# Optimization experiments

Measured on AMD Instinct MI355X. Metric: run time of the kernel, lower is better.

Reference implementation:

```python
import jax, jax.numpy as jnp
import numpy as np

NEG_SLOPE = 0.01  # torch F.leaky_relu default

def leaky_relu(x):
    return jnp.where(x >= 0, x, NEG_SLOPE * x)

def setup_inputs() -> dict:
    key = jax.random.key(0)
    ks = jax.random.split(key, 16)
    N, D, H, L = 2048, 512, 256, 16
    # normalized-adjacency-like matrix: row sums ~0.5 to keep activations sane
    A_hat = jax.random.uniform(ks[0], (N, N), dtype=jnp.float32) / N
    X = jax.random.normal(ks[1], (N, D), dtype=jnp.float32)
    eps = jax.random.normal(ks[2], (N, L), dtype=jnp.float32)
    def lin(k, fan_out, fan_in):
        s = 1.0 / np.sqrt(fan_in)
        kw, kb = jax.random.split(k)
        W = jax.random.uniform(kw, (fan_out, fan_in), minval=-s, maxval=s, dtype=jnp.float32)
        b = jax.random.uniform(kb, (fan_out,), minval=-s, maxval=s, dtype=jnp.float32)
        return W, b
    W1, b1 = lin(ks[3], H, D)          # gcn1
    Wmu, bmu = lin(ks[4], L, H)        # gcn2_mu
    Wlv, blv = lin(ks[5], L, H)        # gcn2_logvar
    Wd1, bd1 = lin(ks[6], 2 * L, 2 * L)  # decoder_fc1
    Wd2, bd2 = lin(ks[7], 1, 2 * L)      # decoder_fc2
    return {"A_hat": A_hat, "X": X, "eps": eps,
            "W1": W1, "b1": b1, "Wmu": Wmu, "bmu": bmu,
            "Wlv": Wlv, "blv": blv, "Wd1": Wd1, "bd1": bd1,
            "Wd2": Wd2, "bd2": bd2}

def reference(A_hat, X, eps, W1, b1, Wmu, bmu, Wlv, blv, Wd1, bd1, Wd2, bd2):
    L = Wmu.shape[0]
    # --- encode: two GCN layers (A_hat @ X) @ W.T + b ---
    Hh = leaky_relu((A_hat @ X) @ W1.T + b1)           # [N, H]
    AH = A_hat @ Hh                                    # [N, H]
    mu = AH @ Wmu.T + bmu                              # [N, L]
    logvar = AH @ Wlv.T + blv                          # [N, L]
    # --- reparameterize ---
    Z = mu + eps * jnp.exp(0.5 * logvar)               # [N, L]
    # --- decode: pairwise MLP on concat(Z_i, Z_j), vectorized ---
    # fc1(concat(Zi,Zj)) = Zi @ Wd1[:, :L].T + Zj @ Wd1[:, L:].T + bd1
    P = Z @ Wd1[:, :L].T                               # [N, 2L]
    Q = Z @ Wd1[:, L:].T                               # [N, 2L]
    h = leaky_relu(P[:, None, :] + Q[None, :, :] + bd1)  # [N, N, 2L]
    A_pred = jax.nn.sigmoid(jnp.einsum('nmh,h->nm', h, Wd2[0]) + bd2[0])  # [N, N]
    return (A_pred, mu, logvar)
```

## Files before the change

kernel.cpp:

```cpp
#include <hip/hip_runtime.h>

#define NNODE 2048
#define DD    512
#define HHID  256
#define LLAT  16
#define H2    32

typedef __attribute__((ext_vector_type(8))) short  short8;
typedef __attribute__((ext_vector_type(4))) float  f32x4;

__device__ __forceinline__ unsigned short f2bf(float x) {
    unsigned int u = __float_as_uint(x);
    unsigned int r = (u + 0x7fffu + ((u >> 16) & 1u)) >> 16;
    return (unsigned short)r;
}
__device__ __forceinline__ float bf2f(unsigned short u) {
    return __uint_as_float(((unsigned int)u) << 16);
}

__global__ __launch_bounds__(256) void t0_cvt(const float* __restrict__ A,
                                              const float* __restrict__ X,
                                              const float* __restrict__ W1,
                                              unsigned short* __restrict__ Abf,
                                              unsigned short* __restrict__ Xbf,
                                              unsigned short* __restrict__ W1bf) {
    const int NT = 1343488;
    for (int v = blockIdx.x * 256 + threadIdx.x; v < NT; v += gridDim.x * 256) {
        const float* src; unsigned short* dst; int off;
        if (v < 1048576)      { src = A;  dst = Abf;  off = v; }
        else if (v < 1310720) { src = X;  dst = Xbf;  off = v - 1048576; }
        else                  { src = W1; dst = W1bf; off = v - 1310720; }
        float4 f = ((const float4*)src)[off];
        short4 h;
        h.x = (short)f2bf(f.x); h.y = (short)f2bf(f.y);
        h.z = (short)f2bf(f.z); h.w = (short)f2bf(f.w);
        ((short4*)dst)[off] = h;
    }
}

__global__ __launch_bounds__(256) void t1_mfma(const unsigned short* __restrict__ W1bf,
                                               const unsigned short* __restrict__ Xbf,
                                               float* __restrict__ XWp) {
    __shared__ __align__(16) unsigned short Ab[64][40];
    __shared__ __align__(16) unsigned short Bb[64][40];
    const int tid = threadIdx.x;
    const int n0 = blockIdx.x * 64;
    const int h0 = blockIdx.y * 64;
    const int ks = blockIdx.z;
    const int lane = tid & 63, wave = tid >> 6;
    const int wm = wave >> 1, wn = wave & 1;
    const int lm = lane & 15, lk = (lane >> 4) * 8;
    const int sr = tid >> 2, sc = (tid & 3) * 8;
    f32x4 acc[2][2] = {};
    for (int it = 0; it < 4; ++it) {
        int kk = ks * 128 + it * 32;
        *(uint4*)&Ab[sr][sc] = *(const uint4*)(W1bf + (size_t)(h0 + sr) * DD + kk + sc);
        *(uint4*)&Bb[sr][sc] = *(const uint4*)(Xbf  + (size_t)(n0 + sr) * DD + kk + sc);
        __syncthreads();
        short8 a0 = *(const short8*)&Ab[wm * 32 + lm][lk];
        short8 a1 = *(const short8*)&Ab[wm * 32 + 16 + lm][lk];
        short8 b0 = *(const short8*)&Bb[wn * 32 + lm][lk];
        short8 b1 = *(const short8*)&Bb[wn * 32 + 16 + lm][lk];
        acc[0][0] = __builtin_amdgcn_mfma_f32_16x16x32_bf16(a0, b0, acc[0][0], 0, 0, 0);
        acc[0][1] = __builtin_amdgcn_mfma_f32_16x16x32_bf16(a0, b1, acc[0][1], 0, 0, 0);
        acc[1][0] = __builtin_amdgcn_mfma_f32_16x16x32_bf16(a1, b0, acc[1][0], 0, 0, 0);
        acc[1][1] = __builtin_amdgcn_mfma_f32_16x16x32_bf16(a1, b1, acc[1][1], 0, 0, 0);
        __syncthreads();
    }
    float* outp = XWp + (size_t)ks * 524288;
    #pragma unroll
    for (int mi = 0; mi < 2; ++mi)
        #pragma unroll
        for (int ni = 0; ni < 2; ++ni)
            #pragma unroll
            for (int r = 0; r < 4; ++r) {
                int row = h0 + wm * 32 + mi * 16 + (lane >> 4) * 4 + r;
                int col = n0 + wn * 32 + ni * 16 + lm;
                outp[(size_t)row * NNODE + col] = acc[mi][ni][r];
            }
}

__global__ __launch_bounds__(256) void t1r(const float* __restrict__ XWp,
                                           unsigned short* __restrict__ XWt) {
    int v = blockIdx.x * 256 + threadIdx.x;
    const float4* p = (const float4*)XWp;
    float4 a = p[v];
    float4 b = p[v + 131072];
    float4 c = p[v + 262144];
    float4 d = p[v + 393216];
    float4 s;
    s.x = (a.x + b.x) + (c.x + d.x);
    s.y = (a.y + b.y) + (c.y + d.y);
    s.z = (a.z + b.z) + (c.z + d.z);
    s.w = (a.w + b.w) + (c.w + d.w);
    short4 h;
    h.x = (short)f2bf(s.x); h.y = (short)f2bf(s.y);
    h.z = (short)f2bf(s.z); h.w = (short)f2bf(s.w);
    ((short4*)XWt)[v] = h;
}

__global__ __launch_bounds__(256) void t2_mfma(const unsigned short* __restrict__ Abf,
                                               const unsigned short* __restrict__ XWt,
                                               float* __restrict__ Hp) {
    __shared__ __align__(16) unsigned short Ab[64][40];
    __shared__ __align__(16) unsigned short Bb[64][40];
    const int tid = threadIdx.x;
    const int m0 = blockIdx.x * 64;
    const int n0 = blockIdx.y * 64;
    const int ks = blockIdx.z;
    const int lane = tid & 63, wave = tid >> 6;
    const int wm = wave >> 1, wn = wave & 1;
    const int lm = lane & 15, lk = (lane >> 4) * 8;
    const int sr = tid >> 2, sc = (tid & 3) * 8;
    f32x4 acc[2][2] = {};
    for (int it = 0; it < 16; ++it) {
        int kk = ks * 512 + it * 32;
        *(uint4*)&Ab[sr][sc] = *(const uint4*)(Abf + (size_t)(m0 + sr) * NNODE + kk + sc);
        *(uint4*)&Bb[sr][sc] = *(const uint4*)(XWt + (size_t)(n0 + sr) * NNODE + kk + sc);
        __syncthreads();
        short8 a0 = *(const short8*)&Ab[wm * 32 + lm][lk];
        short8 a1 = *(const short8*)&Ab[wm * 32 + 16 + lm][lk];
        short8 b0 = *(const short8*)&Bb[wn * 32 + lm][lk];
        short8 b1 = *(const short8*)&Bb[wn * 32 + 16 + lm][lk];
        acc[0][0] = __builtin_amdgcn_mfma_f32_16x16x32_bf16(a0, b0, acc[0][0], 0, 0, 0);
        acc[0][1] = __builtin_amdgcn_mfma_f32_16x16x32_bf16(a0, b1, acc[0][1], 0, 0, 0);
        acc[1][0] = __builtin_amdgcn_mfma_f32_16x16x32_bf16(a1, b0, acc[1][0], 0, 0, 0);
        acc[1][1] = __builtin_amdgcn_mfma_f32_16x16x32_bf16(a1, b1, acc[1][1], 0, 0, 0);
        __syncthreads();
    }
    float* outp = Hp + (size_t)ks * 524288;
    #pragma unroll
    for (int mi = 0; mi < 2; ++mi)
        #pragma unroll
        for (int ni = 0; ni < 2; ++ni)
            #pragma unroll
            for (int r = 0; r < 4; ++r) {
                int row = m0 + wm * 32 + mi * 16 + (lane >> 4) * 4 + r;
                int col = n0 + wn * 32 + ni * 16 + lm;
                outp[(size_t)row * HHID + col] = acc[mi][ni][r];
            }
}

__global__ __launch_bounds__(256) void t2r(const float* __restrict__ Hp,
                                           const float* __restrict__ b1,
                                           unsigned short* __restrict__ Hbf) {
    int v = blockIdx.x * 256 + threadIdx.x;
    const float4* p = (const float4*)Hp;
    float4 a = p[v];
    float4 b = p[v + 131072];
    float4 c = p[v + 262144];
    float4 d = p[v + 393216];
    int dcol = (v & 63) * 4;
    float4 bb = *(const float4*)(b1 + dcol);
    float4 s;
    s.x = (a.x + b.x) + (c.x + d.x) + bb.x;
    s.y = (a.y + b.y) + (c.y + d.y) + bb.y;
    s.z = (a.z + b.z) + (c.z + d.z) + bb.z;
    s.w = (a.w + b.w) + (c.w + d.w) + bb.w;
    s.x = fmaxf(s.x, 0.01f * s.x);
    s.y = fmaxf(s.y, 0.01f * s.y);
    s.z = fmaxf(s.z, 0.01f * s.z);
    s.w = fmaxf(s.w, 0.01f * s.w);
    short4 h;
    h.x = (short)f2bf(s.x); h.y = (short)f2bf(s.y);
    h.z = (short)f2bf(s.z); h.w = (short)f2bf(s.w);
    ((short4*)Hbf)[v] = h;
}

__global__ __launch_bounds__(256) void t3_g(const unsigned short* __restrict__ Hbf,
                                            const float* __restrict__ Wmu,
                                            const float* __restrict__ Wlv,
                                            unsigned short* __restrict__ Gt) {
    __shared__ float Hs[8][260];
    __shared__ float Ws[32][260];
    const int tid = threadIdx.x;
    const int n0 = blockIdx.x * 8;
    #pragma unroll
    for (int s = 0; s < 8; ++s) {
        int idx = tid + s * 256;
        int row = idx >> 6, c = (idx & 63) * 4;
        const float* src = (row < 16) ? (Wmu + (size_t)row * HHID)
                                      : (Wlv + (size_t)(row - 16) * HHID);
        *(float4*)&Ws[row][c] = *(const float4*)(src + c);
    }
    {
        int r = tid >> 5, seg = tid & 31;
        int d = seg * 8;
        ushort4 u0 = *(const ushort4*)(Hbf + (size_t)(n0 + r) * HHID + d);
        ushort4 u1 = *(const ushort4*)(Hbf + (size_t)(n0 + r) * HHID + d + 4);
        Hs[r][d + 0] = bf2f(u0.x); Hs[r][d + 1] = bf2f(u0.y);
        Hs[r][d + 2] = bf2f(u0.z); Hs[r][d + 3] = bf2f(u0.w);
        Hs[r][d + 4] = bf2f(u1.x); Hs[r][d + 5] = bf2f(u1.y);
        Hs[r][d + 6] = bf2f(u1.z); Hs[r][d + 7] = bf2f(u1.w);
    }
    __syncthreads();
    const int r = tid >> 5, j = tid & 31;
    float acc = 0.f;
    #pragma unroll 8
    for (int d4 = 0; d4 < 64; ++d4) {
        float4 a = *(const float4*)&Hs[r][d4 * 4];
        float4 b = *(const float4*)&Ws[j][d4 * 4];
        acc += a.x * b.x + a.y * b.y + a.z * b.z + a.w * b.w;
    }
    Gt[(size_t)j * NNODE + n0 + r] = f2bf(acc);
}

__global__ __launch_bounds__(256) void t4_mfma(const unsigned short* __restrict__ Abf,
                                               const unsigned short* __restrict__ Gt,
                                               float* __restrict__ Mp) {
    __shared__ __align__(16) unsigned short Ab[64][40];
    __shared__ __align__(16) unsigned short Bb[32][40];
    const int tid = threadIdx.x;
    const int m0 = blockIdx.x * 64;
    const int ks = blockIdx.y;
    const int lane = tid & 63, wave = tid >> 6;
    const int lm = lane & 15, lk = (lane >> 4) * 8;
    const int sr = tid >> 2, sc = (tid & 3) * 8;
    f32x4 acc[2] = {};
    for (int it = 0; it < 8; ++it) {
        int kk = ks * 256 + it * 32;
        *(uint4*)&Ab[sr][sc] = *(const uint4*)(Abf + (size_t)(m0 + sr) * NNODE + kk + sc);
        if (tid < 128) {
            int row = tid >> 2, c = (tid & 3) * 8;
            *(uint4*)&Bb[row][c] = *(const uint4*)(Gt + (size_t)row * NNODE + kk + c);
        }
        __syncthreads();
        short8 a  = *(const short8*)&Ab[wave * 16 + lm][lk];
        short8 b0 = *(const short8*)&Bb[lm][lk];
        short8 b1 = *(const short8*)&Bb[16 + lm][lk];
        acc[0] = __builtin_amdgcn_mfma_f32_16x16x32_bf16(a, b0, acc[0], 0, 0, 0);
        acc[1] = __builtin_amdgcn_mfma_f32_16x16x32_bf16(a, b1, acc[1], 0, 0, 0);
        __syncthreads();
    }
    float* outp = Mp + (size_t)ks * 65536;
    #pragma unroll
    for (int ni = 0; ni < 2; ++ni)
        #pragma unroll
        for (int r = 0; r < 4; ++r) {
            int row = m0 + wave * 16 + (lane >> 4) * 4 + r;
            int col = ni * 16 + lm;
            outp[(size_t)row * H2 + col] = acc[ni][r];
        }
}

__global__ __launch_bounds__(256) void t5_z(const float* __restrict__ Mp,
                                            const float* __restrict__ bmu,
                                            const float* __restrict__ blv,
                                            const float* __restrict__ eps,
                                            const float* __restrict__ Wd1,
                                            const float* __restrict__ bd1,
                                            const float* __restrict__ Wd2,
                                            float* __restrict__ out_mu,
                                            float* __restrict__ out_lv,
                                            float* __restrict__ Pp,
                                            float* __restrict__ Qq,
                                            float* __restrict__ WP,
                                            float* __restrict__ WQ) {
    __shared__ float Zs[16][16];
    __shared__ float Psh[16][32];
    __shared__ float Qsh[16][32];
    const int tid = threadIdx.x;
    const int n0 = blockIdx.x * 16;
    {
        int nl = tid >> 4, l = tid & 15;
        int n = n0 + nl;
        float m = bmu[l], lv = blv[l];
        #pragma unroll
        for (int s = 0; s < 8; ++s) {
            m  += Mp[(size_t)s * 65536 + (size_t)n * H2 + l];
            lv += Mp[(size_t)s * 65536 + (size_t)n * H2 + 16 + l];
        }
        out_mu[(size_t)n * LLAT + l] = m;
        out_lv[(size_t)n * LLAT + l] = lv;
        Zs[nl][l] = m + eps[(size_t)n * LLAT + l] * __expf(0.5f * lv);
    }
    __syncthreads();
    #pragma unroll
    for (int p = 0; p < 2; ++p) {
        int idx = tid + p * 256;
        int nl = idx >> 5, o = idx & 31;
        int n = n0 + nl;
        float ap = bd1[o], aq = 0.f;
        #pragma unroll
        for (int l = 0; l < 16; ++l) {
            float z = Zs[nl][l];
            ap = fmaf(z, Wd1[o * H2 + l],      ap);
            aq = fmaf(z, Wd1[o * H2 + 16 + l], aq);
        }
        Pp[(size_t)n * H2 + o] = ap;
        Qq[(size_t)n * H2 + o] = aq;
        Psh[nl][o] = ap;
        Qsh[nl][o] = aq;
    }
    __syncthreads();
    if (tid < 32) {
        int nl = tid & 15, sel = tid >> 4;
        float a = 0.f;
        if (sel == 0) {
            #pragma unroll
            for (int o = 0; o < 32; ++o) a = fmaf(Wd2[o], Psh[nl][o], a);
            WP[n0 + nl] = a;
        } else {
            #pragma unroll
            for (int o = 0; o < 32; ++o) a = fmaf(Wd2[o], Qsh[nl][o], a);
            WQ[n0 + nl] = a;
        }
    }
}

__global__ __launch_bounds__(256) void t6_dec(const float* __restrict__ Pp,
                                              const float* __restrict__ Qq,
                                              const float* __restrict__ WP,
                                              const float* __restrict__ WQ,
                                              const float* __restrict__ Wd2,
                                              const float* __restrict__ bd2,
                                              float* __restrict__ Apred) {
    __shared__ float Qt[32][68];
    __shared__ float Ws2[32];
    __shared__ float WQs[64];
    const int tid = threadIdx.x;
    const int j0 = blockIdx.x * 64, i0 = blockIdx.y * 16;
    #pragma unroll
    for (int s = 0; s < 8; ++s) {
        int idx = tid + s * 256;
        int j = idx >> 5, o = idx & 31;
        Qt[o][j] = Qq[(size_t)(j0 + j) * H2 + o];
    }
    if (tid < 32) Ws2[tid] = Wd2[tid];
    if (tid >= 64 && tid < 128) WQs[tid - 64] = WQ[j0 + tid - 64];
    const int i = i0 + (tid >> 4);
    const int jq = tid & 15;
    float p[32];
    const float4* P4 = (const float4*)(Pp + (size_t)i * H2);
    #pragma unroll
    for (int c = 0; c < 8; ++c) {
        float4 v = P4[c];
        p[c * 4] = v.x; p[c * 4 + 1] = v.y; p[c * 4 + 2] = v.z; p[c * 4 + 3] = v.w;
    }
    const float WPi = WP[i];
    __syncthreads();
    f32x4 acc = {0.f, 0.f, 0.f, 0.f};
    #pragma unroll
    for (int o = 0; o < 32; ++o) {
        float4 q = *(const float4*)&Qt[o][jq * 4];
        float w = Ws2[o], po = p[o];
        acc[0] = fmaf(w, fabsf(po + q.x), acc[0]);
        acc[1] = fmaf(w, fabsf(po + q.y), acc[1]);
        acc[2] = fmaf(w, fabsf(po + q.z), acc[2]);
        acc[3] = fmaf(w, fabsf(po + q.w), acc[3]);
    }
    float4 wq = *(const float4*)&WQs[jq * 4];
    const float base = fmaf(0.505f, WPi, bd2[0]);
    float4 r;
    float l0 = fmaf(0.505f, wq.x, fmaf(0.495f, acc[0], base));
    float l1 = fmaf(0.505f, wq.y, fmaf(0.495f, acc[1], base));
    float l2 = fmaf(0.505f, wq.z, fmaf(0.495f, acc[2], base));
    float l3 = fmaf(0.505f, wq.w, fmaf(0.495f, acc[3], base));
    r.x = 1.f / (1.f + __expf(-l0));
    r.y = 1.f / (1.f + __expf(-l1));
    r.z = 1.f / (1.f + __expf(-l2));
    r.w = 1.f / (1.f + __expf(-l3));
    *(float4*)(Apred + (size_t)i * NNODE + j0 + jq * 4) = r;
}

extern "C" void kernel_launch(void* const* d_in, const int* in_sizes, int n_in,
                              void* d_out, int out_size, void* d_ws, size_t ws_size,
                              hipStream_t stream) {
    const float* A   = (const float*)d_in[0];
    const float* X   = (const float*)d_in[1];
    const float* eps = (const float*)d_in[2];
    const float* W1  = (const float*)d_in[3];
    const float* b1  = (const float*)d_in[4];
    const float* Wmu = (const float*)d_in[5];
    const float* bmu = (const float*)d_in[6];
    const float* Wlv = (const float*)d_in[7];
    const float* blv = (const float*)d_in[8];
    const float* Wd1 = (const float*)d_in[9];
    const float* bd1 = (const float*)d_in[10];
    const float* Wd2 = (const float*)d_in[11];
    const float* bd2 = (const float*)d_in[12];
    float* out = (float*)d_out;
    char* ws = (char*)d_ws;

    unsigned short* Abf  = (unsigned short*)(ws);
    unsigned short* Xbf  = (unsigned short*)(ws + 8388608);
    unsigned short* W1bf = (unsigned short*)(ws + 10485760);
    float*          XWp  = (float*)(ws + 10747904);
    unsigned short* XWt  = (unsigned short*)(ws + 19136512);
    float*          Hp   = (float*)(ws + 20185088);
    unsigned short* Hbf  = (unsigned short*)(ws + 28573696);
    unsigned short* Gt   = (unsigned short*)(ws + 29622272);
    float*          Mp   = (float*)(ws + 29753344);
    float*          Pp   = (float*)(ws + 31850496);
    float*          Qq   = (float*)(ws + 32112640);
    float*          WP   = (float*)(ws + 32374784);
    float*          WQ   = (float*)(ws + 32382976);

    float* out_mu = out + (size_t)NNODE * NNODE;
    float* out_lv = out_mu + NNODE * LLAT;

    t0_cvt <<<2048,            256, 0, stream>>>(A, X, W1, Abf, Xbf, W1bf);
    t1_mfma<<<dim3(32, 4, 4),  256, 0, stream>>>(W1bf, Xbf, XWp);
    t1r    <<<512,             256, 0, stream>>>(XWp, XWt);
    t2_mfma<<<dim3(32, 4, 4),  256, 0, stream>>>(Abf, XWt, Hp);
    t2r    <<<512,             256, 0, stream>>>(Hp, b1, Hbf);
    t3_g   <<<256,             256, 0, stream>>>(Hbf, Wmu, Wlv, Gt);
    t4_mfma<<<dim3(32, 8),     256, 0, stream>>>(Abf, Gt, Mp);
    t5_z   <<<128,             256, 0, stream>>>(Mp, bmu, blv, eps, Wd1, bd1, Wd2,
                                                 out_mu, out_lv, Pp, Qq, WP, WQ);
    t6_dec <<<dim3(32, 128),   256, 0, stream>>>(Pp, Qq, WP, WQ, Wd2, bd2, out);
}
```

Baseline: 141.2 us.

## Fuse conversion into GEMMs, drop split-K reductions, add register prefetch

The X and W1 bf16 conversion is folded into the X·W1 GEMM, which now runs without split-K and writes bf16 XWt directly. The A conversion runs in extra blocks of the same launch. The second GEMM now covers the full K range with 64-wide k-steps and applies bias plus leaky-relu in its epilogue, so the partial-sum buffers and the t1r/t2r reduction kernels go away. Global loads in k2_h and k4_m are prefetched into registers one step ahead. This cuts three launches and several MB of fp32 partial traffic, at the cost of fewer blocks per GEMM and therefore lower parallelism.

```diff
diff --git a/kernel.cpp b/kernel.cpp
--- a/kernel.cpp
+++ b/kernel.cpp
@@ -18,44 +18,53 @@
     return __uint_as_float(((unsigned int)u) << 16);
 }
 
-__global__ __launch_bounds__(256) void t0_cvt(const float* __restrict__ A,
-                                              const float* __restrict__ X,
-                                              const float* __restrict__ W1,
-                                              unsigned short* __restrict__ Abf,
-                                              unsigned short* __restrict__ Xbf,
-                                              unsigned short* __restrict__ W1bf) {
-    const int NT = 1343488;
-    for (int v = blockIdx.x * 256 + threadIdx.x; v < NT; v += gridDim.x * 256) {
-        const float* src; unsigned short* dst; int off;
-        if (v < 1048576)      { src = A;  dst = Abf;  off = v; }
-        else if (v < 1310720) { src = X;  dst = Xbf;  off = v - 1048576; }
-        else                  { src = W1; dst = W1bf; off = v - 1310720; }
-        float4 f = ((const float4*)src)[off];
-        short4 h;
-        h.x = (short)f2bf(f.x); h.y = (short)f2bf(f.y);
-        h.z = (short)f2bf(f.z); h.w = (short)f2bf(f.w);
-        ((short4*)dst)[off] = h;
-    }
-}
-
-__global__ __launch_bounds__(256) void t1_mfma(const unsigned short* __restrict__ W1bf,
-                                               const unsigned short* __restrict__ Xbf,
-                                               float* __restrict__ XWp) {
+__global__ __launch_bounds__(256) void k1_cvt_xw(const float* __restrict__ A,
+                                                 const float* __restrict__ X,
+                                                 const float* __restrict__ W1,
+                                                 unsigned short* __restrict__ Abf,
+                                                 unsigned short* __restrict__ XWt) {
+    const int tid = threadIdx.x;
+    if (blockIdx.x >= 128) {
+        for (int v = (blockIdx.x - 128) * 256 + tid; v < 1048576; v += 32768) {
+            float4 f = ((const float4*)A)[v];
+            short4 h;
+            h.x = (short)f2bf(f.x); h.y = (short)f2bf(f.y);
+            h.z = (short)f2bf(f.z); h.w = (short)f2bf(f.w);
+            ((short4*)Abf)[v] = h;
+        }
+        return;
+    }
     __shared__ __align__(16) unsigned short Ab[64][40];
     __shared__ __align__(16) unsigned short Bb[64][40];
-    const int tid = threadIdx.x;
-    const int n0 = blockIdx.x * 64;
-    const int h0 = blockIdx.y * 64;
-    const int ks = blockIdx.z;
+    const int h0 = (blockIdx.x & 3) * 64;
+    const int n0 = (blockIdx.x >> 2) * 64;
     const int lane = tid & 63, wave = tid >> 6;
     const int wm = wave >> 1, wn = wave & 1;
     const int lm = lane & 15, lk = (lane >> 4) * 8;
     const int sr = tid >> 2, sc = (tid & 3) * 8;
     f32x4 acc[2][2] = {};
-    for (int it = 0; it < 4; ++it) {
-        int kk = ks * 128 + it * 32;
-        *(uint4*)&Ab[sr][sc] = *(const uint4*)(W1bf + (size_t)(h0 + sr) * DD + kk + sc);
-        *(uint4*)&Bb[sr][sc] = *(const uint4*)(Xbf  + (size_t)(n0 + sr) * DD + kk + sc);
+    for (int it = 0; it < 16; ++it) {
+        int kk = it * 32;
+        {
+            const float* ap = W1 + (size_t)(h0 + sr) * DD + kk + sc;
+            float4 f0 = *(const float4*)ap;
+            float4 f1 = *(const float4*)(ap + 4);
+            short8 h;
+            h[0] = (short)f2bf(f0.x); h[1] = (short)f2bf(f0.y);
+            h[2] = (short)f2bf(f0.z); h[3] = (short)f2bf(f0.w);
+            h[4] = (short)f2bf(f1.x); h[5] = (short)f2bf(f1.y);
+            h[6] = (short)f2bf(f1.z); h[7] = (short)f2bf(f1.w);
+            *(short8*)&Ab[sr][sc] = h;
+            const float* bp = X + (size_t)(n0 + sr) * DD + kk + sc;
+            float4 g0 = *(const float4*)bp;
+            float4 g1 = *(const float4*)(bp + 4);
+            short8 g;
+            g[0] = (short)f2bf(g0.x); g[1] = (short)f2bf(g0.y);
+            g[2] = (short)f2bf(g0.z); g[3] = (short)f2bf(g0.w);
+            g[4] = (short)f2bf(g1.x); g[5] = (short)f2bf(g1.y);
+            g[6] = (short)f2bf(g1.z); g[7] = (short)f2bf(g1.w);
+            *(short8*)&Bb[sr][sc] = g;
+        }
         __syncthreads();
         short8 a0 = *(const short8*)&Ab[wm * 32 + lm][lk];
         short8 a1 = *(const short8*)&Ab[wm * 32 + 16 + lm][lk];
@@ -67,7 +76,6 @@
         acc[1][1] = __builtin_amdgcn_mfma_f32_16x16x32_bf16(a1, b1, acc[1][1], 0, 0, 0);
         __syncthreads();
     }
-    float* outp = XWp + (size_t)ks * 524288;
     #pragma unroll
     for (int mi = 0; mi < 2; ++mi)
         #pragma unroll
@@ -76,95 +84,63 @@
             for (int r = 0; r < 4; ++r) {
                 int row = h0 + wm * 32 + mi * 16 + (lane >> 4) * 4 + r;
                 int col = n0 + wn * 32 + ni * 16 + lm;
-                outp[(size_t)row * NNODE + col] = acc[mi][ni][r];
+                XWt[(size_t)row * NNODE + col] = f2bf(acc[mi][ni][r]);
             }
 }
 
-__global__ __launch_bounds__(256) void t1r(const float* __restrict__ XWp,
-                                           unsigned short* __restrict__ XWt) {
-    int v = blockIdx.x * 256 + threadIdx.x;
-    const float4* p = (const float4*)XWp;
-    float4 a = p[v];
-    float4 b = p[v + 131072];
-    float4 c = p[v + 262144];
-    float4 d = p[v + 393216];
-    float4 s;
-    s.x = (a.x + b.x) + (c.x + d.x);
-    s.y = (a.y + b.y) + (c.y + d.y);
-    s.z = (a.z + b.z) + (c.z + d.z);
-    s.w = (a.w + b.w) + (c.w + d.w);
-    short4 h;
-    h.x = (short)f2bf(s.x); h.y = (short)f2bf(s.y);
-    h.z = (short)f2bf(s.z); h.w = (short)f2bf(s.w);
-    ((short4*)XWt)[v] = h;
-}
-
-__global__ __launch_bounds__(256) void t2_mfma(const unsigned short* __restrict__ Abf,
-                                               const unsigned short* __restrict__ XWt,
-                                               float* __restrict__ Hp) {
-    __shared__ __align__(16) unsigned short Ab[64][40];
-    __shared__ __align__(16) unsigned short Bb[64][40];
+__global__ __launch_bounds__(256) void k2_h(const unsigned short* __restrict__ Abf,
+                                            const unsigned short* __restrict__ XWt,
+                                            const float* __restrict__ bias1,
+                                            unsigned short* __restrict__ Hbf) {
+    __shared__ __align__(16) unsigned short Ab[64][72];
+    __shared__ __align__(16) unsigned short Bb[32][72];
     const int tid = threadIdx.x;
     const int m0 = blockIdx.x * 64;
-    const int n0 = blockIdx.y * 64;
-    const int ks = blockIdx.z;
+    const int h0 = blockIdx.y * 32;
     const int lane = tid & 63, wave = tid >> 6;
-    const int wm = wave >> 1, wn = wave & 1;
     const int lm = lane & 15, lk = (lane >> 4) * 8;
-    const int sr = tid >> 2, sc = (tid & 3) * 8;
-    f32x4 acc[2][2] = {};
-    for (int it = 0; it < 16; ++it) {
-        int kk = ks * 512 + it * 32;
-        *(uint4*)&Ab[sr][sc] = *(const uint4*)(Abf + (size_t)(m0 + sr) * NNODE + kk + sc);
-        *(uint4*)&Bb[sr][sc] = *(const uint4*)(XWt + (size_t)(n0 + sr) * NNODE + kk + sc);
-        __syncthreads();
-        short8 a0 = *(const short8*)&Ab[wm * 32 + lm][lk];
-        short8 a1 = *(const short8*)&Ab[wm * 32 + 16 + lm][lk];
-        short8 b0 = *(const short8*)&Bb[wn * 32 + lm][lk];
-        short8 b1 = *(const short8*)&Bb[wn * 32 + 16 + lm][lk];
-        acc[0][0] = __builtin_amdgcn_mfma_f32_16x16x32_bf16(a0, b0, acc[0][0], 0, 0, 0);
-        acc[0][1] = __builtin_amdgcn_mfma_f32_16x16x32_bf16(a0, b1, acc[0][1], 0, 0, 0);
-        acc[1][0] = __builtin_amdgcn_mfma_f32_16x16x32_bf16(a1, b0, acc[1][0], 0, 0, 0);
-        acc[1][1] = __builtin_amdgcn_mfma_f32_16x16x32_bf16(a1, b1, acc[1][1], 0, 0, 0);
-        __syncthreads();
-    }
-    float* outp = Hp + (size_t)ks * 524288;
-    #pragma unroll
-    for (int mi = 0; mi < 2; ++mi)
-        #pragma unroll
-        for (int ni = 0; ni < 2; ++ni)
-            #pragma unroll
-            for (int r = 0; r < 4; ++r) {
-                int row = m0 + wm * 32 + mi * 16 + (lane >> 4) * 4 + r;
-                int col = n0 + wn * 32 + ni * 16 + lm;
-                outp[(size_t)row * HHID + col] = acc[mi][ni][r];
-            }
-}
-
-__global__ __launch_bounds__(256) void t2r(const float* __restrict__ Hp,
-                                           const float* __restrict__ b1,
-                                           unsigned short* __restrict__ Hbf) {
-    int v = blockIdx.x * 256 + threadIdx.x;
-    const float4* p = (const float4*)Hp;
-    float4 a = p[v];
-    float4 b = p[v + 131072];
-    float4 c = p[v + 262144];
-    float4 d = p[v + 393216];
-    int dcol = (v & 63) * 4;
-    float4 bb = *(const float4*)(b1 + dcol);
-    float4 s;
-    s.x = (a.x + b.x) + (c.x + d.x) + bb.x;
-    s.y = (a.y + b.y) + (c.y + d.y) + bb.y;
-    s.z = (a.z + b.z) + (c.z + d.z) + bb.z;
-    s.w = (a.w + b.w) + (c.w + d.w) + bb.w;
-    s.x = fmaxf(s.x, 0.01f * s.x);
-    s.y = fmaxf(s.y, 0.01f * s.y);
-    s.z = fmaxf(s.z, 0.01f * s.z);
-    s.w = fmaxf(s.w, 0.01f * s.w);
-    short4 h;
-    h.x = (short)f2bf(s.x); h.y = (short)f2bf(s.y);
-    h.z = (short)f2bf(s.z); h.w = (short)f2bf(s.w);
-    ((short4*)Hbf)[v] = h;
+    const int sr = tid >> 2, sc = (tid & 3) * 16;
+    const int br = tid >> 3, bc = (tid & 7) * 8;
+    f32x4 acc[2] = {};
+    const unsigned short* aA = Abf + (size_t)(m0 + sr) * NNODE + sc;
+    const unsigned short* aB = XWt + (size_t)(h0 + br) * NNODE + bc;
+    uint4 ra0 = *(const uint4*)(aA);
+    uint4 ra1 = *(const uint4*)(aA + 8);
+    uint4 rb  = *(const uint4*)(aB);
+    for (int it = 0; it < 32; ++it) {
+        *(uint4*)&Ab[sr][sc]     = ra0;
+        *(uint4*)&Ab[sr][sc + 8] = ra1;
+        *(uint4*)&Bb[br][bc]     = rb;
+        __syncthreads();
+        if (it < 31) {
+            int kk = (it + 1) * 64;
+            ra0 = *(const uint4*)(aA + kk);
+            ra1 = *(const uint4*)(aA + kk + 8);
+            rb  = *(const uint4*)(aB + kk);
+        }
+        #pragma unroll
+        for (int ko = 0; ko < 2; ++ko) {
+            short8 a  = *(const short8*)&Ab[wave * 16 + lm][ko * 32 + lk];
+            short8 b0 = *(const short8*)&Bb[lm][ko * 32 + lk];
+            short8 b1 = *(const short8*)&Bb[16 + lm][ko * 32 + lk];
+            acc[0] = __builtin_amdgcn_mfma_f32_16x16x32_bf16(a, b0, acc[0], 0, 0, 0);
+            acc[1] = __builtin_amdgcn_mfma_f32_16x16x32_bf16(a, b1, acc[1], 0, 0, 0);
+        }
+        __syncthreads();
+    }
+    const int q = lane >> 4;
+    #pragma unroll
+    for (int ni = 0; ni < 2; ++ni) {
+        int col = h0 + ni * 16 + lm;
+        float bb = bias1[col];
+        #pragma unroll
+        for (int r = 0; r < 4; ++r) {
+            int row = m0 + wave * 16 + q * 4 + r;
+            float s = acc[ni][r] + bb;
+            s = fmaxf(s, 0.01f * s);
+            Hbf[(size_t)row * HHID + col] = f2bf(s);
+        }
+    }
 }
 
 __global__ __launch_bounds__(256) void t3_g(const unsigned short* __restrict__ Hbf,
@@ -205,9 +181,9 @@
     Gt[(size_t)j * NNODE + n0 + r] = f2bf(acc);
 }
 
-__global__ __launch_bounds__(256) void t4_mfma(const unsigned short* __restrict__ Abf,
-                                               const unsigned short* __restrict__ Gt,
-                                               float* __restrict__ Mp) {
+__global__ __launch_bounds__(256) void k4_m(const unsigned short* __restrict__ Abf,
+                                            const unsigned short* __restrict__ Gt,
+                                            float* __restrict__ Mp) {
     __shared__ __align__(16) unsigned short Ab[64][40];
     __shared__ __align__(16) unsigned short Bb[32][40];
     const int tid = threadIdx.x;
@@ -217,14 +193,23 @@
     const int lm = lane & 15, lk = (lane >> 4) * 8;
     const int sr = tid >> 2, sc = (tid & 3) * 8;
     f32x4 acc[2] = {};
+    const int kbase = ks * 256;
+    const unsigned short* aA = Abf + (size_t)(m0 + sr) * NNODE + kbase + sc;
+    const unsigned short* aB = Gt;
+    uint4 ra = *(const uint4*)aA;
+    uint4 rb = {};
+    if (tid < 128) {
+        aB = Gt + (size_t)(tid >> 2) * NNODE + kbase + (tid & 3) * 8;
+        rb = *(const uint4*)aB;
+    }
     for (int it = 0; it < 8; ++it) {
-        int kk = ks * 256 + it * 32;
-        *(uint4*)&Ab[sr][sc] = *(const uint4*)(Abf + (size_t)(m0 + sr) * NNODE + kk + sc);
-        if (tid < 128) {
-            int row = tid >> 2, c = (tid & 3) * 8;
-            *(uint4*)&Bb[row][c] = *(const uint4*)(Gt + (size_t)row * NNODE + kk + c);
-        }
-        __syncthreads();
+        *(uint4*)&Ab[sr][sc] = ra;
+        if (tid < 128) *(uint4*)&Bb[tid >> 2][(tid & 3) * 8] = rb;
+        __syncthreads();
+        if (it < 7) {
+            ra = *(const uint4*)(aA + (it + 1) * 32);
+            if (tid < 128) rb = *(const uint4*)(aB + (it + 1) * 32);
+        }
         short8 a  = *(const short8*)&Ab[wave * 16 + lm][lk];
         short8 b0 = *(const short8*)&Bb[lm][lk];
         short8 b1 = *(const short8*)&Bb[16 + lm][lk];
@@ -382,31 +367,24 @@
     float* out = (float*)d_out;
     char* ws = (char*)d_ws;
 
-    unsigned short* Abf  = (unsigned short*)(ws);
-    unsigned short* Xbf  = (unsigned short*)(ws + 8388608);
-    unsigned short* W1bf = (unsigned short*)(ws + 10485760);
-    float*          XWp  = (float*)(ws + 10747904);
-    unsigned short* XWt  = (unsigned short*)(ws + 19136512);
-    float*          Hp   = (float*)(ws + 20185088);
-    unsigned short* Hbf  = (unsigned short*)(ws + 28573696);
-    unsigned short* Gt   = (unsigned short*)(ws + 29622272);
-    float*          Mp   = (float*)(ws + 29753344);
-    float*          Pp   = (float*)(ws + 31850496);
-    float*          Qq   = (float*)(ws + 32112640);
-    float*          WP   = (float*)(ws + 32374784);
-    float*          WQ   = (float*)(ws + 32382976);
+    unsigned short* Abf = (unsigned short*)(ws);
+    unsigned short* XWt = (unsigned short*)(ws + 8388608);
+    unsigned short* Hbf = (unsigned short*)(ws + 9437184);
+    unsigned short* Gt  = (unsigned short*)(ws + 10485760);
+    float*          Mp  = (float*)(ws + 10616832);
+    float*          Pp  = (float*)(ws + 12713984);
+    float*          Qq  = (float*)(ws + 12976128);
+    float*          WP  = (float*)(ws + 13238272);
+    float*          WQ  = (float*)(ws + 13246464);
 
     float* out_mu = out + (size_t)NNODE * NNODE;
     float* out_lv = out_mu + NNODE * LLAT;
 
-    t0_cvt <<<2048,            256, 0, stream>>>(A, X, W1, Abf, Xbf, W1bf);
-    t1_mfma<<<dim3(32, 4, 4),  256, 0, stream>>>(W1bf, Xbf, XWp);
-    t1r    <<<512,             256, 0, stream>>>(XWp, XWt);
-    t2_mfma<<<dim3(32, 4, 4),  256, 0, stream>>>(Abf, XWt, Hp);
-    t2r    <<<512,             256, 0, stream>>>(Hp, b1, Hbf);
-    t3_g   <<<256,             256, 0, stream>>>(Hbf, Wmu, Wlv, Gt);
-    t4_mfma<<<dim3(32, 8),     256, 0, stream>>>(Abf, Gt, Mp);
-    t5_z   <<<128,             256, 0, stream>>>(Mp, bmu, blv, eps, Wd1, bd1, Wd2,
+    k1_cvt_xw<<<256,           256, 0, stream>>>(A, X, W1, Abf, XWt);
+    k2_h     <<<dim3(32, 8),   256, 0, stream>>>(Abf, XWt, b1, Hbf);
+    t3_g     <<<256,           256, 0, stream>>>(Hbf, Wmu, Wlv, Gt);
+    k4_m     <<<dim3(32, 8),   256, 0, stream>>>(Abf, Gt, Mp);
+    t5_z     <<<128,           256, 0, stream>>>(Mp, bmu, blv, eps, Wd1, bd1, Wd2,
                                                  out_mu, out_lv, Pp, Qq, WP, WQ);
-    t6_dec <<<dim3(32, 128),   256, 0, stream>>>(Pp, Qq, WP, WQ, Wd2, bd2, out);
-}
+    t6_dec   <<<dim3(32, 128), 256, 0, stream>>>(Pp, Qq, WP, WQ, Wd2, bd2, out);
+}
```

Result: slower. 150.0 us (+6.3%).

## Fuse split-K reductions into GEMM kernels via last-block atomic counters

Applied to the files above, without the earlier changes.

Removes the separate split-K reduction kernels (t1r, t2r, t5_z) by having each GEMM tile's last-arriving K-split block, detected with an atomic counter, sum the partials and apply the epilogue. Counters are zeroed in the conversion kernel, and partials are written and read with agent-scope atomic stores and loads. This saves three kernel launches and some global round trips. In exchange it adds fences and atomics, serialises the epilogue onto one block per tile, and uses scalar rather than vectorised loads in the reduction.

```diff
diff --git a/kernel.cpp b/kernel.cpp
--- a/kernel.cpp
+++ b/kernel.cpp
@@ -17,13 +17,24 @@
 __device__ __forceinline__ float bf2f(unsigned short u) {
     return __uint_as_float(((unsigned int)u) << 16);
 }
+__device__ __forceinline__ void stg_agent(float* p, float v) {
+    __hip_atomic_store(p, v, __ATOMIC_RELAXED, __HIP_MEMORY_SCOPE_AGENT);
+}
+__device__ __forceinline__ float ldg_agent(const float* p) {
+    return __hip_atomic_load(p, __ATOMIC_RELAXED, __HIP_MEMORY_SCOPE_AGENT);
+}
 
 __global__ __launch_bounds__(256) void t0_cvt(const float* __restrict__ A,
                                               const float* __restrict__ X,
                                               const float* __restrict__ W1,
                                               unsigned short* __restrict__ Abf,
                                               unsigned short* __restrict__ Xbf,
-                                              unsigned short* __restrict__ W1bf) {
+                                              unsigned short* __restrict__ W1bf,
+                                              unsigned int* __restrict__ cnt) {
+    if (blockIdx.x == 0) {
+        cnt[threadIdx.x] = 0u;
+        if (threadIdx.x < 32) cnt[256 + threadIdx.x] = 0u;
+    }
     const int NT = 1343488;
     for (int v = blockIdx.x * 256 + threadIdx.x; v < NT; v += gridDim.x * 256) {
         const float* src; unsigned short* dst; int off;
@@ -38,11 +49,14 @@
     }
 }
 
-__global__ __launch_bounds__(256) void t1_mfma(const unsigned short* __restrict__ W1bf,
-                                               const unsigned short* __restrict__ Xbf,
-                                               float* __restrict__ XWp) {
+__global__ __launch_bounds__(256) void t1f(const unsigned short* __restrict__ W1bf,
+                                           const unsigned short* __restrict__ Xbf,
+                                           float* __restrict__ XWp,
+                                           unsigned short* __restrict__ XWt,
+                                           unsigned int* __restrict__ cnt) {
     __shared__ __align__(16) unsigned short Ab[64][40];
     __shared__ __align__(16) unsigned short Bb[64][40];
+    __shared__ unsigned int lastf;
     const int tid = threadIdx.x;
     const int n0 = blockIdx.x * 64;
     const int h0 = blockIdx.y * 64;
@@ -76,34 +90,46 @@
             for (int r = 0; r < 4; ++r) {
                 int row = h0 + wm * 32 + mi * 16 + (lane >> 4) * 4 + r;
                 int col = n0 + wn * 32 + ni * 16 + lm;
-                outp[(size_t)row * NNODE + col] = acc[mi][ni][r];
+                stg_agent(&outp[(size_t)row * NNODE + col], acc[mi][ni][r]);
             }
-}
-
-__global__ __launch_bounds__(256) void t1r(const float* __restrict__ XWp,
-                                           unsigned short* __restrict__ XWt) {
-    int v = blockIdx.x * 256 + threadIdx.x;
-    const float4* p = (const float4*)XWp;
-    float4 a = p[v];
-    float4 b = p[v + 131072];
-    float4 c = p[v + 262144];
-    float4 d = p[v + 393216];
-    float4 s;
-    s.x = (a.x + b.x) + (c.x + d.x);
-    s.y = (a.y + b.y) + (c.y + d.y);
-    s.z = (a.z + b.z) + (c.z + d.z);
-    s.w = (a.w + b.w) + (c.w + d.w);
-    short4 h;
-    h.x = (short)f2bf(s.x); h.y = (short)f2bf(s.y);
-    h.z = (short)f2bf(s.z); h.w = (short)f2bf(s.w);
-    ((short4*)XWt)[v] = h;
-}
-
-__global__ __launch_bounds__(256) void t2_mfma(const unsigned short* __restrict__ Abf,
-                                               const unsigned short* __restrict__ XWt,
-                                               float* __restrict__ Hp) {
+    __syncthreads();
+    if (tid == 0) {
+        __threadfence();
+        lastf = (atomicAdd(&cnt[blockIdx.y * 32 + blockIdx.x], 1u) == 3u) ? 1u : 0u;
+    }
+    __syncthreads();
+    if (!lastf) return;
+    __threadfence();
+    const int rr = h0 + (tid >> 2);
+    const int c0 = n0 + (tid & 3) * 16;
+    const float* base = XWp + (size_t)rr * NNODE + c0;
+    #pragma unroll
+    for (int q = 0; q < 4; ++q) {
+        float s4[4];
+        #pragma unroll
+        for (int e = 0; e < 4; ++e) {
+            float a = ldg_agent(base + q * 4 + e);
+            float b = ldg_agent(base + 524288 + q * 4 + e);
+            float c = ldg_agent(base + 1048576 + q * 4 + e);
+            float d = ldg_agent(base + 1572864 + q * 4 + e);
+            s4[e] = (a + b) + (c + d);
+        }
+        short4 h;
+        h.x = (short)f2bf(s4[0]); h.y = (short)f2bf(s4[1]);
+        h.z = (short)f2bf(s4[2]); h.w = (short)f2bf(s4[3]);
+        *(short4*)(XWt + (size_t)rr * NNODE + c0 + q * 4) = h;
+    }
+}
+
+__global__ __launch_bounds__(256) void t2f(const unsigned short* __restrict__ Abf,
+                                           const unsigned short* __restrict__ XWt,
+                                           float* __restrict__ Hp,
+                                           const float* __restrict__ bias1,
+                                           unsigned short* __restrict__ Hbf,
+                                           unsigned int* __restrict__ cnt) {
     __shared__ __align__(16) unsigned short Ab[64][40];
     __shared__ __align__(16) unsigned short Bb[64][40];
+    __shared__ unsigned int lastf;
     const int tid = threadIdx.x;
     const int m0 = blockIdx.x * 64;
     const int n0 = blockIdx.y * 64;
@@ -137,34 +163,36 @@
             for (int r = 0; r < 4; ++r) {
                 int row = m0 + wm * 32 + mi * 16 + (lane >> 4) * 4 + r;
                 int col = n0 + wn * 32 + ni * 16 + lm;
-                outp[(size_t)row * HHID + col] = acc[mi][ni][r];
+                stg_agent(&outp[(size_t)row * HHID + col], acc[mi][ni][r]);
             }
-}
-
-__global__ __launch_bounds__(256) void t2r(const float* __restrict__ Hp,
-                                           const float* __restrict__ b1,
-                                           unsigned short* __restrict__ Hbf) {
-    int v = blockIdx.x * 256 + threadIdx.x;
-    const float4* p = (const float4*)Hp;
-    float4 a = p[v];
-    float4 b = p[v + 131072];
-    float4 c = p[v + 262144];
-    float4 d = p[v + 393216];
-    int dcol = (v & 63) * 4;
-    float4 bb = *(const float4*)(b1 + dcol);
-    float4 s;
-    s.x = (a.x + b.x) + (c.x + d.x) + bb.x;
-    s.y = (a.y + b.y) + (c.y + d.y) + bb.y;
-    s.z = (a.z + b.z) + (c.z + d.z) + bb.z;
-    s.w = (a.w + b.w) + (c.w + d.w) + bb.w;
-    s.x = fmaxf(s.x, 0.01f * s.x);
-    s.y = fmaxf(s.y, 0.01f * s.y);
-    s.z = fmaxf(s.z, 0.01f * s.z);
-    s.w = fmaxf(s.w, 0.01f * s.w);
-    short4 h;
-    h.x = (short)f2bf(s.x); h.y = (short)f2bf(s.y);
-    h.z = (short)f2bf(s.z); h.w = (short)f2bf(s.w);
-    ((short4*)Hbf)[v] = h;
+    __syncthreads();
+    if (tid == 0) {
+        __threadfence();
+        lastf = (atomicAdd(&cnt[128 + blockIdx.y * 32 + blockIdx.x], 1u) == 3u) ? 1u : 0u;
+    }
+    __syncthreads();
+    if (!lastf) return;
+    __threadfence();
+    const int rr = m0 + (tid >> 2);
+    const int c0 = n0 + (tid & 3) * 16;
+    const float* base = Hp + (size_t)rr * HHID + c0;
+    #pragma unroll
+    for (int q = 0; q < 4; ++q) {
+        float s4[4];
+        #pragma unroll
+        for (int e = 0; e < 4; ++e) {
+            float a = ldg_agent(base + q * 4 + e);
+            float b = ldg_agent(base + 524288 + q * 4 + e);
+            float c = ldg_agent(base + 1048576 + q * 4 + e);
+            float d = ldg_agent(base + 1572864 + q * 4 + e);
+            float s = (a + b) + (c + d) + bias1[c0 + q * 4 + e];
+            s4[e] = fmaxf(s, 0.01f * s);
+        }
+        short4 h;
+        h.x = (short)f2bf(s4[0]); h.y = (short)f2bf(s4[1]);
+        h.z = (short)f2bf(s4[2]); h.w = (short)f2bf(s4[3]);
+        *(short4*)(Hbf + (size_t)rr * HHID + c0 + q * 4) = h;
+    }
 }
 
 __global__ __launch_bounds__(256) void t3_g(const unsigned short* __restrict__ Hbf,
@@ -205,11 +233,28 @@
     Gt[(size_t)j * NNODE + n0 + r] = f2bf(acc);
 }
 
-__global__ __launch_bounds__(256) void t4_mfma(const unsigned short* __restrict__ Abf,
-                                               const unsigned short* __restrict__ Gt,
-                                               float* __restrict__ Mp) {
+__global__ __launch_bounds__(256) void t4f(const unsigned short* __restrict__ Abf,
+                                           const unsigned short* __restrict__ Gt,
+                                           float* __restrict__ Mp,
+                                           unsigned int* __restrict__ cnt,
+                                           const float* __restrict__ bmu,
+                                           const float* __restrict__ blv,
+                                           const float* __restrict__ eps,
+                                           const float* __restrict__ Wd1,
+                                           const float* __restrict__ bd1,
+                                           const float* __restrict__ Wd2,
+                                           float* __restrict__ out_mu,
+                                           float* __restrict__ out_lv,
+                                           float* __restrict__ Pp,
+                                           float* __restrict__ Qq,
+                                           float* __restrict__ WP,
+                                           float* __restrict__ WQ) {
     __shared__ __align__(16) unsigned short Ab[64][40];
     __shared__ __align__(16) unsigned short Bb[32][40];
+    __shared__ float Zs[64][16];
+    __shared__ float Psh[64][32];
+    __shared__ float Qsh[64][32];
+    __shared__ unsigned int lastf;
     const int tid = threadIdx.x;
     const int m0 = blockIdx.x * 64;
     const int ks = blockIdx.y;
@@ -239,36 +284,26 @@
         for (int r = 0; r < 4; ++r) {
             int row = m0 + wave * 16 + (lane >> 4) * 4 + r;
             int col = ni * 16 + lm;
-            outp[(size_t)row * H2 + col] = acc[ni][r];
-        }
-}
-
-__global__ __launch_bounds__(256) void t5_z(const float* __restrict__ Mp,
-                                            const float* __restrict__ bmu,
-                                            const float* __restrict__ blv,
-                                            const float* __restrict__ eps,
-                                            const float* __restrict__ Wd1,
-                                            const float* __restrict__ bd1,
-                                            const float* __restrict__ Wd2,
-                                            float* __restrict__ out_mu,
-                                            float* __restrict__ out_lv,
-                                            float* __restrict__ Pp,
-                                            float* __restrict__ Qq,
-                                            float* __restrict__ WP,
-                                            float* __restrict__ WQ) {
-    __shared__ float Zs[16][16];
-    __shared__ float Psh[16][32];
-    __shared__ float Qsh[16][32];
-    const int tid = threadIdx.x;
-    const int n0 = blockIdx.x * 16;
-    {
-        int nl = tid >> 4, l = tid & 15;
-        int n = n0 + nl;
+            stg_agent(&outp[(size_t)row * H2 + col], acc[ni][r]);
+        }
+    __syncthreads();
+    if (tid == 0) {
+        __threadfence();
+        lastf = (atomicAdd(&cnt[256 + blockIdx.x], 1u) == 7u) ? 1u : 0u;
+    }
+    __syncthreads();
+    if (!lastf) return;
+    __threadfence();
+    #pragma unroll
+    for (int p = 0; p < 4; ++p) {
+        int idx = tid + p * 256;
+        int nl = idx >> 4, l = idx & 15;
+        int n = m0 + nl;
         float m = bmu[l], lv = blv[l];
         #pragma unroll
         for (int s = 0; s < 8; ++s) {
-            m  += Mp[(size_t)s * 65536 + (size_t)n * H2 + l];
-            lv += Mp[(size_t)s * 65536 + (size_t)n * H2 + 16 + l];
+            m  += ldg_agent(&Mp[(size_t)s * 65536 + (size_t)n * H2 + l]);
+            lv += ldg_agent(&Mp[(size_t)s * 65536 + (size_t)n * H2 + 16 + l]);
         }
         out_mu[(size_t)n * LLAT + l] = m;
         out_lv[(size_t)n * LLAT + l] = lv;
@@ -276,10 +311,10 @@
     }
     __syncthreads();
     #pragma unroll
-    for (int p = 0; p < 2; ++p) {
+    for (int p = 0; p < 8; ++p) {
         int idx = tid + p * 256;
         int nl = idx >> 5, o = idx & 31;
-        int n = n0 + nl;
+        int n = m0 + nl;
         float ap = bd1[o], aq = 0.f;
         #pragma unroll
         for (int l = 0; l < 16; ++l) {
@@ -293,17 +328,17 @@
         Qsh[nl][o] = aq;
     }
     __syncthreads();
-    if (tid < 32) {
-        int nl = tid & 15, sel = tid >> 4;
+    if (tid < 128) {
+        int nl = tid & 63, sel = tid >> 6;
         float a = 0.f;
         if (sel == 0) {
             #pragma unroll
             for (int o = 0; o < 32; ++o) a = fmaf(Wd2[o], Psh[nl][o], a);
-            WP[n0 + nl] = a;
+            WP[m0 + nl] = a;
         } else {
             #pragma unroll
             for (int o = 0; o < 32; ++o) a = fmaf(Wd2[o], Qsh[nl][o], a);
-            WQ[n0 + nl] = a;
+            WQ[m0 + nl] = a;
         }
     }
 }
@@ -395,18 +430,17 @@
     float*          Qq   = (float*)(ws + 32112640);
     float*          WP   = (float*)(ws + 32374784);
     float*          WQ   = (float*)(ws + 32382976);
+    unsigned int*   cnt  = (unsigned int*)(ws + 32391168);
 
     float* out_mu = out + (size_t)NNODE * NNODE;
     float* out_lv = out_mu + NNODE * LLAT;
 
-    t0_cvt <<<2048,            256, 0, stream>>>(A, X, W1, Abf, Xbf, W1bf);
-    t1_mfma<<<dim3(32, 4, 4),  256, 0, stream>>>(W1bf, Xbf, XWp);
-    t1r    <<<512,             256, 0, stream>>>(XWp, XWt);
-    t2_mfma<<<dim3(32, 4, 4),  256, 0, stream>>>(Abf, XWt, Hp);
-    t2r    <<<512,             256, 0, stream>>>(Hp, b1, Hbf);
-    t3_g   <<<256,             256, 0, stream>>>(Hbf, Wmu, Wlv, Gt);
-    t4_mfma<<<dim3(32, 8),     256, 0, stream>>>(Abf, Gt, Mp);
-    t5_z   <<<128,             256, 0, stream>>>(Mp, bmu, blv, eps, Wd1, bd1, Wd2,
-                                                 out_mu, out_lv, Pp, Qq, WP, WQ);
-    t6_dec <<<dim3(32, 128),   256, 0, stream>>>(Pp, Qq, WP, WQ, Wd2, bd2, out);
-}
+    t0_cvt<<<2048,           256, 0, stream>>>(A, X, W1, Abf, Xbf, W1bf, cnt);
+    t1f   <<<dim3(32, 4, 4), 256, 0, stream>>>(W1bf, Xbf, XWp, XWt, cnt);
+    t2f   <<<dim3(32, 4, 4), 256, 0, stream>>>(Abf, XWt, Hp, b1, Hbf, cnt);
+    t3_g  <<<256,            256, 0, stream>>>(Hbf, Wmu, Wlv, Gt);
+    t4f   <<<dim3(32, 8),    256, 0, stream>>>(Abf, Gt, Mp, cnt, bmu, blv, eps,
+                                               Wd1, bd1, Wd2, out_mu, out_lv,
+                                               Pp, Qq, WP, WQ);
+    t6_dec<<<dim3(32, 128),  256, 0, stream>>>(Pp, Qq, WP, WQ, Wd2, bd2, out);
+}
```

New measurement: 205.0 us. 1.45x slower.
